# Kernel tuning notes

Measured on AMD Instinct MI355X. Metric: run time of the kernel, lower is better.

The kernel has to match this reference:

```python
import jax, jax.numpy as jnp
import numpy as np

B, L, H, O, C = 64, 32, 128, 16384, 32


def setup_inputs() -> dict:
    key = jax.random.key(0)
    ks = jax.random.split(key, 8)
    s = lambda k, shp, fan: jax.random.normal(k, shp, jnp.float32) / np.sqrt(fan)
    return {
        "z": jax.random.normal(ks[0], (B, L), jnp.float32),
        "feature_embedding": jax.random.normal(ks[1], (O, C), jnp.float32),
        "feature_bias": jax.random.normal(ks[2], (O, 1), jnp.float32),
        "Wz": s(ks[3], (L, H), L),
        "bz": jnp.zeros((H,), jnp.float32),
        "W1": s(ks[4], (H + C + 1, H), H + C + 1),
        "b1": jnp.zeros((H,), jnp.float32),
        "W2": s(ks[5], (H, 1), H),
        "b2": jnp.zeros((1,), jnp.float32),
    }


def reference(z, feature_embedding, feature_bias, Wz, bz, W1, b1, W2, b2):
    # z_processor: Linear + ReLU (dropout_rate=0)
    pz = jax.nn.relu(z @ Wz + bz)  # [B, H]
    # concat([pz, F, b], -1) @ W1  ==  pz@W1_h + F@W1_f + b*W1_b  (no [B,O,H+C+1] materialization)
    W1_h, W1_f, W1_b = W1[:H], W1[H:H + C], W1[H + C:]  # [H,H],[C,H],[1,H]
    h = jax.nn.relu(
        (pz @ W1_h)[:, None, :]                    # [B,1,H]
        + (feature_embedding @ W1_f)[None, :, :]   # [1,O,H]
        + feature_bias * W1_b                      # [O,H] broadcast
        + b1
    )  # [B, O, H]
    out = jnp.einsum("boh,ho->bo", h, W2) + b2  # [B, O]
    return out
```

## Files before the change

### kernel.cpp

```cpp
#include <hip/hip_runtime.h>

#define Bb 64
#define Ll 32
#define Hh 128
#define Oo 16384
#define Cc 32


__global__ __launch_bounds__(256) void prep_kernel(
    const float* __restrict__ z, const float* __restrict__ Wz,
    const float* __restrict__ bz, const float* __restrict__ W1,
    const float* __restrict__ b1, const float* __restrict__ W2,
    const float* __restrict__ b2,
    float* __restrict__ A, float* __restrict__ SA2w,
    float* __restrict__ w2h, float* __restrict__ w1t,
    float* __restrict__ gcoef)
{
    __shared__ float pz[2][Hh];
    __shared__ float ps[2][Hh];
    const int t  = threadIdx.x;
    const int h  = t & (Hh - 1);
    const int bb = t >> 7;
    const int b  = blockIdx.x * 2 + bb;

    float v = bz[h];
#pragma unroll
    for (int c = 0; c < Ll; ++c)
        v = fmaf(z[b * Ll + c], Wz[c * Hh + h], v);
    pz[bb][h] = fmaxf(v, 0.f);
    __syncthreads();

    float a = 0.f;
#pragma unroll
    for (int k = 0; k < Hh; ++k)
        a = fmaf(pz[bb][k], W1[k * Hh + h], a);
    A[b * Hh + h] = a;
    ps[bb][h] = 0.5f * W2[h] * a;
    __syncthreads();

    if (h == 0) {
        float s = b2[0];
        for (int k = 0; k < Hh; ++k) s += ps[bb][k];
        SA2w[b] = s;
    }

    if (t < 128) {
        const int h2 = blockIdx.x * 4 + (t >> 5);
        const int c  = t & 31;
        w1t[h2 * Cc + c] = W1[(Hh + c) * Hh + h2];
    }
    if (t < 4) {
        const int h2 = blockIdx.x * 4 + t;
        w2h[h2] = 0.5f * W2[h2];
        gcoef[2 * h2 + 0] = W1[(Hh + Cc) * Hh + h2];
        gcoef[2 * h2 + 1] = b1[h2];
    }
}

__global__ __launch_bounds__(256) void g_kernel(
    const float* __restrict__ fe, const float* __restrict__ fb,
    const float* __restrict__ w1t, const float* __restrict__ gcoef,
    float* __restrict__ g_t)
{
    const int t    = threadIdx.x;
    const int lane = t & 63;
    const int wave = __builtin_amdgcn_readfirstlane(t >> 6);
    const int o    = (blockIdx.x & 255) * 64 + lane;
    const int hb   = (blockIdx.x >> 8) * 64 + wave * 16;

    float4 fer[8];
    const float4* fep = (const float4*)(fe + o * Cc);
#pragma unroll
    for (int k = 0; k < 8; ++k) fer[k] = fep[k];
    const float fbv = fb[o];

#pragma unroll 1
    for (int j = 0; j < 8; ++j) {
        const int h = hb + 2 * j;
        const float* __restrict__ wt0 = w1t + (h + 0) * Cc;
        const float* __restrict__ wt1 = w1t + (h + 1) * Cc;
        float g0 = fmaf(fbv, gcoef[2 * h + 0], gcoef[2 * h + 1]);
        float g1 = fmaf(fbv, gcoef[2 * h + 2], gcoef[2 * h + 3]);
#pragma unroll
        for (int k = 0; k < 8; ++k) {
            g0 = fmaf(fer[k].x, wt0[4 * k + 0], g0);
            g0 = fmaf(fer[k].y, wt0[4 * k + 1], g0);
            g0 = fmaf(fer[k].z, wt0[4 * k + 2], g0);
            g0 = fmaf(fer[k].w, wt0[4 * k + 3], g0);
            g1 = fmaf(fer[k].x, wt1[4 * k + 0], g1);
            g1 = fmaf(fer[k].y, wt1[4 * k + 1], g1);
            g1 = fmaf(fer[k].z, wt1[4 * k + 2], g1);
            g1 = fmaf(fer[k].w, wt1[4 * k + 3], g1);
        }
        const int hp = (hb >> 1) + j;
        *(float2*)(g_t + hp * (2 * Oo) + 2 * o) = make_float2(g0, g1);
    }
}

__global__ __launch_bounds__(256) void m_kernel(
    const float* __restrict__ A, const float* __restrict__ SA2w,
    const float* __restrict__ w2h, const float* __restrict__ g_t,
    float* __restrict__ out)
{
    const int t    = threadIdx.x;
    const int lane = t & 63;
    const int wave = __builtin_amdgcn_readfirstlane(t >> 6);
    const int o    = (blockIdx.x & 255) * 64 + lane;
    const int b0   = (blockIdx.x >> 8) * 16 + wave * 4;

    const float* __restrict__ A0 = A + (b0 + 0) * Hh;
    const float* __restrict__ A1 = A + (b0 + 1) * Hh;
    const float* __restrict__ A2 = A + (b0 + 2) * Hh;
    const float* __restrict__ A3 = A + (b0 + 3) * Hh;

    float acc0 = 0.f, acc1 = 0.f, acc2 = 0.f, acc3 = 0.f, sg = 0.f;

#pragma unroll 1
    for (int hc = 0; hc < 16; ++hc) {
        const int h0 = hc * 8;
        float g[8];
#pragma unroll
        for (int k = 0; k < 4; ++k) {
            const float2 g2 = *(const float2*)(g_t + (4 * hc + k) * (2 * Oo) + 2 * o);
            g[2 * k + 0] = g2.x;
            g[2 * k + 1] = g2.y;
        }
#pragma unroll
        for (int j = 0; j < 8; ++j) {
            const int h = h0 + j;
            const float w = w2h[h];
            sg   = fmaf(w, g[j], sg);
            acc0 = fmaf(__builtin_fabsf(A0[h] + g[j]), w, acc0);
            acc1 = fmaf(__builtin_fabsf(A1[h] + g[j]), w, acc1);
            acc2 = fmaf(__builtin_fabsf(A2[h] + g[j]), w, acc2);
            acc3 = fmaf(__builtin_fabsf(A3[h] + g[j]), w, acc3);
        }
    }

    const float s0 = SA2w[b0 + 0], s1 = SA2w[b0 + 1];
    const float s2 = SA2w[b0 + 2], s3 = SA2w[b0 + 3];
    out[(b0 + 0) * Oo + o] = acc0 + sg + s0;
    out[(b0 + 1) * Oo + o] = acc1 + sg + s1;
    out[(b0 + 2) * Oo + o] = acc2 + sg + s2;
    out[(b0 + 3) * Oo + o] = acc3 + sg + s3;
}

extern "C" void kernel_launch(void* const* d_in, const int* in_sizes, int n_in,
                              void* d_out, int out_size, void* d_ws, size_t ws_size,
                              hipStream_t stream) {
    (void)in_sizes; (void)n_in; (void)out_size; (void)ws_size;
    const float* z   = (const float*)d_in[0];
    const float* fe  = (const float*)d_in[1];
    const float* fb  = (const float*)d_in[2];
    const float* Wz  = (const float*)d_in[3];
    const float* bz  = (const float*)d_in[4];
    const float* W1  = (const float*)d_in[5];
    const float* b1  = (const float*)d_in[6];
    const float* W2  = (const float*)d_in[7];
    const float* b2  = (const float*)d_in[8];
    float* out   = (float*)d_out;
    float* A     = (float*)d_ws;
    float* SA2w  = A + Bb * Hh;
    float* w2h   = SA2w + Bb;
    float* w1t   = w2h + Hh;
    float* gcoef = w1t + Hh * Cc;
    float* g_t   = (float*)d_ws + 16384;

    prep_kernel<<<Bb / 2, 256, 0, stream>>>(z, Wz, bz, W1, b1, W2, b2,
                                            A, SA2w, w2h, w1t, gcoef);
    g_kernel<<<512, 256, 0, stream>>>(fe, fb, w1t, gcoef, g_t);
    m_kernel<<<1024, 256, 0, stream>>>(A, SA2w, w2h, g_t, out);
}
```

Measured before the change: 97.29 us.

## Retile m_kernel to two outputs per thread with vectorized A/w2 loads

```diff
diff --git a/kernel.cpp b/kernel.cpp
--- a/kernel.cpp
+++ b/kernel.cpp
@@ -64,7 +64,7 @@
 {
     const int t    = threadIdx.x;
     const int lane = t & 63;
-    const int wave = __builtin_amdgcn_readfirstlane(t >> 6);
+    const int wave = t >> 6;
     const int o    = (blockIdx.x & 255) * 64 + lane;
     const int hb   = (blockIdx.x >> 8) * 64 + wave * 16;
 
@@ -74,7 +74,7 @@
     for (int k = 0; k < 8; ++k) fer[k] = fep[k];
     const float fbv = fb[o];
 
-#pragma unroll 1
+#pragma unroll 2
     for (int j = 0; j < 8; ++j) {
         const int h = hb + 2 * j;
         const float* __restrict__ wt0 = w1t + (h + 0) * Cc;
@@ -92,8 +92,8 @@
             g1 = fmaf(fer[k].z, wt1[4 * k + 2], g1);
             g1 = fmaf(fer[k].w, wt1[4 * k + 3], g1);
         }
-        const int hp = (hb >> 1) + j;
-        *(float2*)(g_t + hp * (2 * Oo) + 2 * o) = make_float2(g0, g1);
+        g_t[(h + 0) * Oo + o] = g0;
+        g_t[(h + 1) * Oo + o] = g1;
     }
 }
 
@@ -102,47 +102,58 @@
     const float* __restrict__ w2h, const float* __restrict__ g_t,
     float* __restrict__ out)
 {
-    const int t    = threadIdx.x;
-    const int lane = t & 63;
-    const int wave = __builtin_amdgcn_readfirstlane(t >> 6);
-    const int o    = (blockIdx.x & 255) * 64 + lane;
-    const int b0   = (blockIdx.x >> 8) * 16 + wave * 4;
+    const int t  = threadIdx.x;
+    const int o  = (blockIdx.x & 31) * 512 + 2 * t;
+    const int b0 = (blockIdx.x >> 5) * 4;
 
     const float* __restrict__ A0 = A + (b0 + 0) * Hh;
     const float* __restrict__ A1 = A + (b0 + 1) * Hh;
     const float* __restrict__ A2 = A + (b0 + 2) * Hh;
     const float* __restrict__ A3 = A + (b0 + 3) * Hh;
 
-    float acc0 = 0.f, acc1 = 0.f, acc2 = 0.f, acc3 = 0.f, sg = 0.f;
+    float acc[4][2];
+#pragma unroll
+    for (int bi = 0; bi < 4; ++bi) { acc[bi][0] = 0.f; acc[bi][1] = 0.f; }
+    float sg0 = 0.f, sg1 = 0.f;
 
-#pragma unroll 1
-    for (int hc = 0; hc < 16; ++hc) {
-        const int h0 = hc * 8;
-        float g[8];
+#pragma unroll 2
+    for (int hc = 0; hc < 32; ++hc) {
+        const int h = 4 * hc;
+        float2 g[4];
 #pragma unroll
-        for (int k = 0; k < 4; ++k) {
-            const float2 g2 = *(const float2*)(g_t + (4 * hc + k) * (2 * Oo) + 2 * o);
-            g[2 * k + 0] = g2.x;
-            g[2 * k + 1] = g2.y;
-        }
+        for (int j = 0; j < 4; ++j)
+            g[j] = *(const float2*)(g_t + (h + j) * Oo + o);
+        const float4 w4 = *(const float4*)(w2h + h);
+        const float4 a0 = *(const float4*)(A0 + h);
+        const float4 a1 = *(const float4*)(A1 + h);
+        const float4 a2 = *(const float4*)(A2 + h);
+        const float4 a3 = *(const float4*)(A3 + h);
 #pragma unroll
-        for (int j = 0; j < 8; ++j) {
-            const int h = h0 + j;
-            const float w = w2h[h];
-            sg   = fmaf(w, g[j], sg);
-            acc0 = fmaf(__builtin_fabsf(A0[h] + g[j]), w, acc0);
-            acc1 = fmaf(__builtin_fabsf(A1[h] + g[j]), w, acc1);
-            acc2 = fmaf(__builtin_fabsf(A2[h] + g[j]), w, acc2);
-            acc3 = fmaf(__builtin_fabsf(A3[h] + g[j]), w, acc3);
+        for (int j = 0; j < 4; ++j) {
+            const float wj  = (&w4.x)[j];
+            const float gx  = g[j].x, gy = g[j].y;
+            sg0 = fmaf(wj, gx, sg0);
+            sg1 = fmaf(wj, gy, sg1);
+            const float e0 = (&a0.x)[j], e1 = (&a1.x)[j];
+            const float e2 = (&a2.x)[j], e3 = (&a3.x)[j];
+            acc[0][0] = fmaf(__builtin_fabsf(e0 + gx), wj, acc[0][0]);
+            acc[0][1] = fmaf(__builtin_fabsf(e0 + gy), wj, acc[0][1]);
+            acc[1][0] = fmaf(__builtin_fabsf(e1 + gx), wj, acc[1][0]);
+            acc[1][1] = fmaf(__builtin_fabsf(e1 + gy), wj, acc[1][1]);
+            acc[2][0] = fmaf(__builtin_fabsf(e2 + gx), wj, acc[2][0]);
+            acc[2][1] = fmaf(__builtin_fabsf(e2 + gy), wj, acc[2][1]);
+            acc[3][0] = fmaf(__builtin_fabsf(e3 + gx), wj, acc[3][0]);
+            acc[3][1] = fmaf(__builtin_fabsf(e3 + gy), wj, acc[3][1]);
         }
     }
 
-    const float s0 = SA2w[b0 + 0], s1 = SA2w[b0 + 1];
-    const float s2 = SA2w[b0 + 2], s3 = SA2w[b0 + 3];
-    out[(b0 + 0) * Oo + o] = acc0 + sg + s0;
-    out[(b0 + 1) * Oo + o] = acc1 + sg + s1;
-    out[(b0 + 2) * Oo + o] = acc2 + sg + s2;
-    out[(b0 + 3) * Oo + o] = acc3 + sg + s3;
+#pragma unroll
+    for (int bi = 0; bi < 4; ++bi) {
+        const float s = SA2w[b0 + bi];
+        const float2 r = make_float2(acc[bi][0] + sg0 + s,
+                                     acc[bi][1] + sg1 + s);
+        *(float2*)(out + (b0 + bi) * Oo + o) = r;
+    }
 }
 
 extern "C" void kernel_launch(void* const* d_in, const int* in_sizes, int n_in,
@@ -169,5 +180,5 @@
     prep_kernel<<<Bb / 2, 256, 0, stream>>>(z, Wz, bz, W1, b1, W2, b2,
                                             A, SA2w, w2h, w1t, gcoef);
     g_kernel<<<512, 256, 0, stream>>>(fe, fb, w1t, gcoef, g_t);
-    m_kernel<<<1024, 256, 0, stream>>>(A, SA2w, w2h, g_t, out);
+    m_kernel<<<512, 256, 0, stream>>>(A, SA2w, w2h, g_t, out);
 }
```

Measured after the change: 105.2 us. 1.08x slower.
